# Kernel tuning notes

Hardware: AMD Instinct MI355X
Metric: run time of the kernel (lower is better)

The kernel has to match this reference:

```python
import jax, jax.numpy as jnp
import numpy as np

EMB = 128
HID = 512
B = 8192
W = 128


def setup_inputs() -> dict:
    key = jax.random.key(0)
    k1, k2, k3, k4, k5, k6, k7 = jax.random.split(key, 7)
    context_info = jax.random.normal(k1, (B, 4 * HID), dtype=jnp.float32)
    window = jax.random.normal(k2, (B, W, EMB), dtype=jnp.float32)
    window_mask = jax.random.bernoulli(k3, 0.9, (B, W))
    # guarantee at least one valid position per row (center is always valid)
    window_mask = window_mask.at[:, W // 2].set(True)
    ctr = jax.random.normal(k4, (B, EMB), dtype=jnp.float32)
    # learned params
    W_bilinear = jax.random.normal(k5, (EMB, EMB), dtype=jnp.float32) / np.sqrt(EMB)  # nn.Bilinear weight [1, emb, emb] squeezed
    W_linear = jax.random.normal(k6, (1, 4 * HID + EMB), dtype=jnp.float32) / np.sqrt(4 * HID + EMB)
    b_linear = jax.random.normal(k7, (1,), dtype=jnp.float32) * 0.01
    return {"context_info": context_info, "window": window, "window_mask": window_mask,
            "ctr": ctr, "W_bilinear": W_bilinear, "W_linear": W_linear, "b_linear": b_linear}


def reference(context_info, window, window_mask, ctr, W_bilinear, W_linear, b_linear):
    # bilinear attention score: ctr^T W window_t  -> [B, W]
    e = jnp.einsum('be,ef,bwf->bw', ctr, W_bilinear, window)
    invalid = jnp.logical_not(window_mask)
    e = jnp.where(invalid, -jnp.inf, e)
    # subtract per-row max (masked_fill of the broadcast max to 0 at invalid slots)
    m = jnp.max(e, axis=1, keepdims=True)            # [B, 1]
    e = e - jnp.where(invalid, 0.0, m)               # broadcast to [B, W]
    at_weights = jax.nn.softmax(e, axis=1)
    at_weights = jnp.where(invalid, 0.0, at_weights)
    # weighted sum over window -> [B, emb]
    context_eos = jnp.einsum('bw,bwe->be', at_weights, window)
    context_full = jnp.concatenate([context_info, context_eos], axis=1)
    logits = context_full @ W_linear.T + b_linear    # [B, 1]
    return logits
```

## Files before the change

kernel.cpp:

```cpp
#include <hip/hip_runtime.h>

#define EMB  128
#define HID4 2048
#define WIN  128

__global__ __launch_bounds__(256) void eos_fused_kernel(
    const float* __restrict__ ci,
    const float* __restrict__ window,
    const unsigned char* __restrict__ mask_raw,
    const float* __restrict__ ctr,
    const float* __restrict__ Wb,
    const float* __restrict__ WL,
    const float* __restrict__ bL,
    float* __restrict__ out)
{
    const int b    = blockIdx.x;
    const int tid  = threadIdx.x;
    const int lane = tid & 63;
    const int wave = tid >> 6;
    const int hl   = lane & 31;
    const int hw   = wave * 2 + (lane >> 5);

    __shared__ float ctr_s[EMB];
    __shared__ float vm_s[WIN];
    __shared__ float pu_s[2][EMB];
    __shared__ float u_s[EMB];
    __shared__ float acc_s[8][EMB];
    __shared__ float z_s[8];
    __shared__ float red_s[4];
    __shared__ unsigned long long det_s[4][2];
    __shared__ int mode_s;

    {
        const unsigned int* mw = (const unsigned int*)mask_raw;
        int hi = 0, nf = 0;
        if (tid < 128) {
            unsigned int v = mw[tid];
            hi = (v & 0xFFFFFF00u) ? 1 : 0;
            nf = (v != 0u && v != 0x3F800000u) ? 1 : 0;
        }
        unsigned long long bh = __ballot(hi);
        unsigned long long bf = __ballot(nf);
        if (lane == 0) { det_s[wave][0] = bh; det_s[wave][1] = bf; }
    }
    if (tid < EMB) ctr_s[tid] = ctr[(size_t)b * EMB + tid];
    __syncthreads();
    if (tid == 0) {
        unsigned long long ah = det_s[0][0] | det_s[1][0] | det_s[2][0] | det_s[3][0];
        unsigned long long af = det_s[0][1] | det_s[1][1] | det_s[2][1] | det_s[3][1];
        mode_s = (af == 0ULL) ? 2 : (ah ? 0 : 1);
    }
    __syncthreads();

    {
        const int mode = mode_s;
        if (tid < WIN) {
            bool valid;
            if (mode == 0)      valid = (mask_raw[(size_t)b * WIN + tid] != 0);
            else if (mode == 1) valid = (((const int*)mask_raw)[(size_t)b * WIN + tid] != 0);
            else                valid = (((const float*)mask_raw)[(size_t)b * WIN + tid] != 0.f);
            vm_s[tid] = valid ? 1.f : 0.f;
        }
    }

    {
        const int f  = tid & (EMB - 1);
        const int h  = tid >> 7;
        const int e0 = h * 64;
        float s = 0.f;
        #pragma unroll 8
        for (int e = 0; e < 64; ++e)
            s = fmaf(ctr_s[e0 + e], Wb[(e0 + e) * EMB + f], s);
        pu_s[h][f] = s;
    }
    __syncthreads();
    if (tid < EMB) u_s[tid] = pu_s[0][tid] + pu_s[1][tid];
    __syncthreads();

    float4 u4;
    u4.x = u_s[hl*4+0]; u4.y = u_s[hl*4+1]; u4.z = u_s[hl*4+2]; u4.w = u_s[hl*4+3];

    const float4* win4 = (const float4*)(window + (size_t)b * WIN * EMB);

    float  Z   = 0.f;
    float4 acc = make_float4(0.f, 0.f, 0.f, 0.f);

    #pragma unroll 4
    for (int i = 0; i < 16; ++i) {
        const int w = i * 8 + hw;
        float4 wv = win4[w * 32 + hl];
        float s = wv.x * u4.x;
        s = fmaf(wv.y, u4.y, s);
        s = fmaf(wv.z, u4.z, s);
        s = fmaf(wv.w, u4.w, s);
        s += __shfl_xor(s, 1);
        s += __shfl_xor(s, 2);
        s += __shfl_xor(s, 4);
        s += __shfl_xor(s, 8);
        s += __shfl_xor(s, 16);
        const float p = vm_s[w] * __expf(s);
        Z += p;
        acc.x = fmaf(p, wv.x, acc.x);
        acc.y = fmaf(p, wv.y, acc.y);
        acc.z = fmaf(p, wv.z, acc.z);
        acc.w = fmaf(p, wv.w, acc.w);
    }

    acc_s[hw][hl*4+0] = acc.x;
    acc_s[hw][hl*4+1] = acc.y;
    acc_s[hw][hl*4+2] = acc.z;
    acc_s[hw][hl*4+3] = acc.w;
    if (hl == 0) z_s[hw] = 0.f;
    __syncthreads();
    if (hl == 0) z_s[hw] = Z;
    __syncthreads();

    const float4* ci4 = (const float4*)(ci + (size_t)b * HID4);
    const float4* wl4 = (const float4*)WL;
    float part;
    {
        float4 c0 = ci4[tid],       w0 = wl4[tid];
        float4 c1 = ci4[tid + 256], w1 = wl4[tid + 256];
        part = c0.x * w0.x;
        part = fmaf(c0.y, w0.y, part);
        part = fmaf(c0.z, w0.z, part);
        part = fmaf(c0.w, w0.w, part);
        part = fmaf(c1.x, w1.x, part);
        part = fmaf(c1.y, w1.y, part);
        part = fmaf(c1.z, w1.z, part);
        part = fmaf(c1.w, w1.w, part);
    }
    if (tid < EMB) {
        float Zt = z_s[0] + z_s[1] + z_s[2] + z_s[3]
                 + z_s[4] + z_s[5] + z_s[6] + z_s[7];
        float a = 0.f;
        #pragma unroll
        for (int p = 0; p < 8; ++p) a += acc_s[p][tid];
        const float ce = a / Zt;
        part = fmaf(ce, WL[HID4 + tid], part);
    }
    part += __shfl_xor(part, 1);
    part += __shfl_xor(part, 2);
    part += __shfl_xor(part, 4);
    part += __shfl_xor(part, 8);
    part += __shfl_xor(part, 16);
    part += __shfl_xor(part, 32);
    if (lane == 0) red_s[wave] = part;
    __syncthreads();
    if (tid == 0)
        out[b] = red_s[0] + red_s[1] + red_s[2] + red_s[3] + bL[0];
}

extern "C" void kernel_launch(void* const* d_in, const int* in_sizes, int n_in,
                              void* d_out, int out_size, void* d_ws, size_t ws_size,
                              hipStream_t stream) {
    const float*         ci     = (const float*)d_in[0];
    const float*         window = (const float*)d_in[1];
    const unsigned char* mask   = (const unsigned char*)d_in[2];
    const float*         ctr    = (const float*)d_in[3];
    const float*         Wb     = (const float*)d_in[4];
    const float*         WL     = (const float*)d_in[5];
    const float*         bL     = (const float*)d_in[6];
    float*               out    = (float*)d_out;

    const int B = in_sizes[0] / HID4;
    hipLaunchKernelGGL(eos_fused_kernel, dim3(B), dim3(256), 0, stream,
                       ci, window, mask, ctr, Wb, WL, bL, out);
}
```

Before: 115.3 us.

## Split ctr·W_bilinear projection and mask decode into batched prep kernel

Moves the per-row u = ctr·W_bilinear projection and mask decoding into a separate prep kernel that handles 8 rows per block, so each W_bilinear load is reused across 8 rows. The results go to workspace. The main kernel then only loads u and the mask floats, issues the context_info loads early, and drops several barriers. It also sets an occupancy hint of 8 blocks per CU. The cost is an extra kernel launch and a workspace round-trip, and the original fused kernel is kept as a fallback when workspace is too small.

```diff
diff --git a/kernel.cpp b/kernel.cpp
--- a/kernel.cpp
+++ b/kernel.cpp
@@ -3,13 +3,81 @@
 #define EMB  128
 #define HID4 2048
 #define WIN  128
-
-__global__ __launch_bounds__(256) void eos_fused_kernel(
+#define BQ   8
+
+__global__ __launch_bounds__(256) void eos_prep_kernel(
+    const float* __restrict__ ctr,
+    const unsigned char* __restrict__ mask_raw,
+    const float* __restrict__ Wb,
+    float* __restrict__ u_out,
+    float* __restrict__ vm_out)
+{
+    const int b0   = blockIdx.x * BQ;
+    const int tid  = threadIdx.x;
+    const int lane = tid & 63;
+    const int wave = tid >> 6;
+
+    __shared__ float ctr_s[BQ][EMB];
+    __shared__ float pu_s[2][BQ * EMB];
+    __shared__ unsigned long long det_s[4][2];
+    __shared__ int mode_s;
+
+    {
+        const unsigned int* mw = (const unsigned int*)mask_raw;
+        int hi = 0, nf = 0;
+        if (tid < 128) {
+            unsigned int v = mw[tid];
+            hi = (v & 0xFFFFFF00u) ? 1 : 0;
+            nf = (v != 0u && v != 0x3F800000u) ? 1 : 0;
+        }
+        unsigned long long bh = __ballot(hi);
+        unsigned long long bf = __ballot(nf);
+        if (lane == 0) { det_s[wave][0] = bh; det_s[wave][1] = bf; }
+    }
+    ((float4*)&ctr_s[0][0])[tid] = ((const float4*)(ctr + (size_t)b0 * EMB))[tid];
+    __syncthreads();
+    if (tid == 0) {
+        unsigned long long ah = det_s[0][0] | det_s[1][0] | det_s[2][0] | det_s[3][0];
+        unsigned long long af = det_s[0][1] | det_s[1][1] | det_s[2][1] | det_s[3][1];
+        mode_s = (af == 0ULL) ? 2 : (ah ? 0 : 1);
+    }
+
+    const int f = tid & 127;
+    const int h = tid >> 7;
+    float acc[BQ];
+    #pragma unroll
+    for (int r = 0; r < BQ; ++r) acc[r] = 0.f;
+    const float* wbp = Wb + (size_t)(h * 64) * EMB + f;
+    #pragma unroll 4
+    for (int e = 0; e < 64; ++e) {
+        const float w = wbp[(size_t)e * EMB];
+        #pragma unroll
+        for (int r = 0; r < BQ; ++r)
+            acc[r] = fmaf(ctr_s[r][h * 64 + e], w, acc[r]);
+    }
+    #pragma unroll
+    for (int r = 0; r < BQ; ++r) pu_s[h][r * EMB + f] = acc[r];
+    __syncthreads();
+
+    for (int idx = tid; idx < BQ * EMB; idx += 256)
+        u_out[(size_t)b0 * EMB + idx] = pu_s[0][idx] + pu_s[1][idx];
+
+    const int mode = mode_s;
+    for (int idx = tid; idx < BQ * WIN; idx += 256) {
+        const size_t gi = (size_t)b0 * WIN + idx;
+        bool valid;
+        if (mode == 0)      valid = (mask_raw[gi] != 0);
+        else if (mode == 1) valid = (((const int*)mask_raw)[gi] != 0);
+        else                valid = (((const float*)mask_raw)[gi] != 0.f);
+        vm_out[gi] = valid ? 1.f : 0.f;
+    }
+}
+
+__global__ __launch_bounds__(256, 8) void eos_main_kernel(
     const float* __restrict__ ci,
     const float* __restrict__ window,
-    const unsigned char* __restrict__ mask_raw,
-    const float* __restrict__ ctr,
-    const float* __restrict__ Wb,
+    const float* __restrict__ u_prep,
+    const float* __restrict__ vm_prep,
     const float* __restrict__ WL,
     const float* __restrict__ bL,
     float* __restrict__ out)
@@ -21,64 +89,17 @@
     const int hl   = lane & 31;
     const int hw   = wave * 2 + (lane >> 5);
 
-    __shared__ float ctr_s[EMB];
     __shared__ float vm_s[WIN];
-    __shared__ float pu_s[2][EMB];
-    __shared__ float u_s[EMB];
     __shared__ float acc_s[8][EMB];
     __shared__ float z_s[8];
     __shared__ float red_s[4];
-    __shared__ unsigned long long det_s[4][2];
-    __shared__ int mode_s;
-
-    {
-        const unsigned int* mw = (const unsigned int*)mask_raw;
-        int hi = 0, nf = 0;
-        if (tid < 128) {
-            unsigned int v = mw[tid];
-            hi = (v & 0xFFFFFF00u) ? 1 : 0;
-            nf = (v != 0u && v != 0x3F800000u) ? 1 : 0;
-        }
-        unsigned long long bh = __ballot(hi);
-        unsigned long long bf = __ballot(nf);
-        if (lane == 0) { det_s[wave][0] = bh; det_s[wave][1] = bf; }
-    }
-    if (tid < EMB) ctr_s[tid] = ctr[(size_t)b * EMB + tid];
-    __syncthreads();
-    if (tid == 0) {
-        unsigned long long ah = det_s[0][0] | det_s[1][0] | det_s[2][0] | det_s[3][0];
-        unsigned long long af = det_s[0][1] | det_s[1][1] | det_s[2][1] | det_s[3][1];
-        mode_s = (af == 0ULL) ? 2 : (ah ? 0 : 1);
-    }
-    __syncthreads();
-
-    {
-        const int mode = mode_s;
-        if (tid < WIN) {
-            bool valid;
-            if (mode == 0)      valid = (mask_raw[(size_t)b * WIN + tid] != 0);
-            else if (mode == 1) valid = (((const int*)mask_raw)[(size_t)b * WIN + tid] != 0);
-            else                valid = (((const float*)mask_raw)[(size_t)b * WIN + tid] != 0.f);
-            vm_s[tid] = valid ? 1.f : 0.f;
-        }
-    }
-
-    {
-        const int f  = tid & (EMB - 1);
-        const int h  = tid >> 7;
-        const int e0 = h * 64;
-        float s = 0.f;
-        #pragma unroll 8
-        for (int e = 0; e < 64; ++e)
-            s = fmaf(ctr_s[e0 + e], Wb[(e0 + e) * EMB + f], s);
-        pu_s[h][f] = s;
-    }
-    __syncthreads();
-    if (tid < EMB) u_s[tid] = pu_s[0][tid] + pu_s[1][tid];
-    __syncthreads();
-
-    float4 u4;
-    u4.x = u_s[hl*4+0]; u4.y = u_s[hl*4+1]; u4.z = u_s[hl*4+2]; u4.w = u_s[hl*4+3];
+
+    const float4* ci4 = (const float4*)(ci + (size_t)b * HID4);
+    float4 c0 = ci4[tid];
+    float4 c1 = ci4[tid + 256];
+    float4 u4 = ((const float4*)(u_prep + (size_t)b * EMB))[hl];
+    if (tid < WIN) vm_s[tid] = vm_prep[(size_t)b * WIN + tid];
+    __syncthreads();
 
     const float4* win4 = (const float4*)(window + (size_t)b * WIN * EMB);
 
@@ -110,8 +131,138 @@
     acc_s[hw][hl*4+1] = acc.y;
     acc_s[hw][hl*4+2] = acc.z;
     acc_s[hw][hl*4+3] = acc.w;
-    if (hl == 0) z_s[hw] = 0.f;
-    __syncthreads();
+    if (hl == 0) z_s[hw] = Z;
+    __syncthreads();
+
+    const float4* wl4 = (const float4*)WL;
+    float4 w0 = wl4[tid], w1 = wl4[tid + 256];
+    float part;
+    part = c0.x * w0.x;
+    part = fmaf(c0.y, w0.y, part);
+    part = fmaf(c0.z, w0.z, part);
+    part = fmaf(c0.w, w0.w, part);
+    part = fmaf(c1.x, w1.x, part);
+    part = fmaf(c1.y, w1.y, part);
+    part = fmaf(c1.z, w1.z, part);
+    part = fmaf(c1.w, w1.w, part);
+
+    if (tid < EMB) {
+        const float Zt = z_s[0] + z_s[1] + z_s[2] + z_s[3]
+                       + z_s[4] + z_s[5] + z_s[6] + z_s[7];
+        float a = 0.f;
+        #pragma unroll
+        for (int p = 0; p < 8; ++p) a += acc_s[p][tid];
+        part = fmaf(a / Zt, WL[HID4 + tid], part);
+    }
+    part += __shfl_xor(part, 1);
+    part += __shfl_xor(part, 2);
+    part += __shfl_xor(part, 4);
+    part += __shfl_xor(part, 8);
+    part += __shfl_xor(part, 16);
+    part += __shfl_xor(part, 32);
+    if (lane == 0) red_s[wave] = part;
+    __syncthreads();
+    if (tid == 0)
+        out[b] = red_s[0] + red_s[1] + red_s[2] + red_s[3] + bL[0];
+}
+
+__global__ __launch_bounds__(256) void eos_fused_fallback(
+    const float* __restrict__ ci, const float* __restrict__ window,
+    const unsigned char* __restrict__ mask_raw, const float* __restrict__ ctr,
+    const float* __restrict__ Wb, const float* __restrict__ WL,
+    const float* __restrict__ bL, float* __restrict__ out)
+{
+    const int b    = blockIdx.x;
+    const int tid  = threadIdx.x;
+    const int lane = tid & 63;
+    const int wave = tid >> 6;
+    const int hl   = lane & 31;
+    const int hw   = wave * 2 + (lane >> 5);
+
+    __shared__ float ctr_s[EMB];
+    __shared__ float vm_s[WIN];
+    __shared__ float pu_s[2][EMB];
+    __shared__ float u_s[EMB];
+    __shared__ float acc_s[8][EMB];
+    __shared__ float z_s[8];
+    __shared__ float red_s[4];
+    __shared__ unsigned long long det_s[4][2];
+    __shared__ int mode_s;
+
+    {
+        const unsigned int* mw = (const unsigned int*)mask_raw;
+        int hi = 0, nf = 0;
+        if (tid < 128) {
+            unsigned int v = mw[tid];
+            hi = (v & 0xFFFFFF00u) ? 1 : 0;
+            nf = (v != 0u && v != 0x3F800000u) ? 1 : 0;
+        }
+        unsigned long long bh = __ballot(hi);
+        unsigned long long bf = __ballot(nf);
+        if (lane == 0) { det_s[wave][0] = bh; det_s[wave][1] = bf; }
+    }
+    if (tid < EMB) ctr_s[tid] = ctr[(size_t)b * EMB + tid];
+    __syncthreads();
+    if (tid == 0) {
+        unsigned long long ah = det_s[0][0] | det_s[1][0] | det_s[2][0] | det_s[3][0];
+        unsigned long long af = det_s[0][1] | det_s[1][1] | det_s[2][1] | det_s[3][1];
+        mode_s = (af == 0ULL) ? 2 : (ah ? 0 : 1);
+    }
+    __syncthreads();
+    {
+        const int mode = mode_s;
+        if (tid < WIN) {
+            bool valid;
+            if (mode == 0)      valid = (mask_raw[(size_t)b * WIN + tid] != 0);
+            else if (mode == 1) valid = (((const int*)mask_raw)[(size_t)b * WIN + tid] != 0);
+            else                valid = (((const float*)mask_raw)[(size_t)b * WIN + tid] != 0.f);
+            vm_s[tid] = valid ? 1.f : 0.f;
+        }
+    }
+    {
+        const int f  = tid & (EMB - 1);
+        const int h  = tid >> 7;
+        const int e0 = h * 64;
+        float s = 0.f;
+        #pragma unroll 8
+        for (int e = 0; e < 64; ++e)
+            s = fmaf(ctr_s[e0 + e], Wb[(e0 + e) * EMB + f], s);
+        pu_s[h][f] = s;
+    }
+    __syncthreads();
+    if (tid < EMB) u_s[tid] = pu_s[0][tid] + pu_s[1][tid];
+    __syncthreads();
+
+    float4 u4;
+    u4.x = u_s[hl*4+0]; u4.y = u_s[hl*4+1]; u4.z = u_s[hl*4+2]; u4.w = u_s[hl*4+3];
+
+    const float4* win4 = (const float4*)(window + (size_t)b * WIN * EMB);
+    float  Z   = 0.f;
+    float4 acc = make_float4(0.f, 0.f, 0.f, 0.f);
+    #pragma unroll 4
+    for (int i = 0; i < 16; ++i) {
+        const int w = i * 8 + hw;
+        float4 wv = win4[w * 32 + hl];
+        float s = wv.x * u4.x;
+        s = fmaf(wv.y, u4.y, s);
+        s = fmaf(wv.z, u4.z, s);
+        s = fmaf(wv.w, u4.w, s);
+        s += __shfl_xor(s, 1);
+        s += __shfl_xor(s, 2);
+        s += __shfl_xor(s, 4);
+        s += __shfl_xor(s, 8);
+        s += __shfl_xor(s, 16);
+        const float p = vm_s[w] * __expf(s);
+        Z += p;
+        acc.x = fmaf(p, wv.x, acc.x);
+        acc.y = fmaf(p, wv.y, acc.y);
+        acc.z = fmaf(p, wv.z, acc.z);
+        acc.w = fmaf(p, wv.w, acc.w);
+    }
+    acc_s[hw][hl*4+0] = acc.x;
+    acc_s[hw][hl*4+1] = acc.y;
+    acc_s[hw][hl*4+2] = acc.z;
+    acc_s[hw][hl*4+3] = acc.w;
     if (hl == 0) z_s[hw] = Z;
     __syncthreads();
 
@@ -131,13 +282,12 @@
         part = fmaf(c1.w, w1.w, part);
     }
     if (tid < EMB) {
-        float Zt = z_s[0] + z_s[1] + z_s[2] + z_s[3]
-                 + z_s[4] + z_s[5] + z_s[6] + z_s[7];
+        const float Zt = z_s[0] + z_s[1] + z_s[2] + z_s[3]
+                       + z_s[4] + z_s[5] + z_s[6] + z_s[7];
         float a = 0.f;
         #pragma unroll
         for (int p = 0; p < 8; ++p) a += acc_s[p][tid];
-        const float ce = a / Zt;
-        part = fmaf(ce, WL[HID4 + tid], part);
+        part = fmaf(a / Zt, WL[HID4 + tid], part);
     }
     part += __shfl_xor(part, 1);
     part += __shfl_xor(part, 2);
@@ -164,6 +314,17 @@
     float*               out    = (float*)d_out;
 
     const int B = in_sizes[0] / HID4;
-    hipLaunchKernelGGL(eos_fused_kernel, dim3(B), dim3(256), 0, stream,
-                       ci, window, mask, ctr, Wb, WL, bL, out);
+    const size_t need = (size_t)B * EMB * sizeof(float) * 2;
+
+    if (ws_size >= need) {
+        float* u_ws  = (float*)d_ws;
+        float* vm_ws = u_ws + (size_t)B * EMB;
+        hipLaunchKernelGGL(eos_prep_kernel, dim3(B / BQ), dim3(256), 0, stream,
+                           ctr, mask, Wb, u_ws, vm_ws);
+        hipLaunchKernelGGL(eos_main_kernel, dim3(B), dim3(256), 0, stream,
+                           ci, window, u_ws, vm_ws, WL, bL, out);
+    } else {
+        hipLaunchKernelGGL(eos_fused_fallback, dim3(B), dim3(256), 0, stream,
+                           ci, window, mask, ctr, Wb, WL, bL, out);
+    }
 }
```

After: 127.9 us. 11.0% more time.

## Map one batch row per wavefront and drop shared-memory reductions

Applied to the files above, without the earlier changes.

Each wavefront now handles a full batch row: it computes the bilinear projection vector itself, keeps mask values in registers read via shuffles, and reduces accumulators with cross-half shuffles instead of shared memory and block barriers. This removes syncthreads and LDS traffic per row. In exchange each wave reads the full Wb matrix (via cache) and runs a longer serial loop over the window, with less parallelism per row.

```diff
diff --git a/kernel.cpp b/kernel.cpp
--- a/kernel.cpp
+++ b/kernel.cpp
@@ -4,7 +4,7 @@
 #define HID4 2048
 #define WIN  128
 
-__global__ __launch_bounds__(256) void eos_fused_kernel(
+__global__ __launch_bounds__(256) void eos_wave_kernel(
     const float* __restrict__ ci,
     const float* __restrict__ window,
     const unsigned char* __restrict__ mask_raw,
@@ -12,83 +12,68 @@
     const float* __restrict__ Wb,
     const float* __restrict__ WL,
     const float* __restrict__ bL,
-    float* __restrict__ out)
+    float* __restrict__ out,
+    int B)
 {
-    const int b    = blockIdx.x;
     const int tid  = threadIdx.x;
     const int lane = tid & 63;
     const int wave = tid >> 6;
     const int hl   = lane & 31;
-    const int hw   = wave * 2 + (lane >> 5);
+    const int h    = lane >> 5;
+    const int row  = blockIdx.x * 4 + wave;
+    if (row >= B) return;
 
-    __shared__ float ctr_s[EMB];
-    __shared__ float vm_s[WIN];
-    __shared__ float pu_s[2][EMB];
-    __shared__ float u_s[EMB];
-    __shared__ float acc_s[8][EMB];
-    __shared__ float z_s[8];
-    __shared__ float red_s[4];
-    __shared__ unsigned long long det_s[4][2];
-    __shared__ int mode_s;
+    int mode;
+    {
+        const unsigned int v = ((const unsigned int*)mask_raw)[lane];
+        const unsigned long long bh = __ballot((v & 0xFFFFFF00u) != 0u);
+        const unsigned long long bf = __ballot(v != 0u && v != 0x3F800000u);
+        mode = (bf == 0ULL) ? 2 : (bh ? 0 : 1);
+    }
 
+    float vm0, vm1;
     {
-        const unsigned int* mw = (const unsigned int*)mask_raw;
-        int hi = 0, nf = 0;
-        if (tid < 128) {
-            unsigned int v = mw[tid];
-            hi = (v & 0xFFFFFF00u) ? 1 : 0;
-            nf = (v != 0u && v != 0x3F800000u) ? 1 : 0;
-        }
-        unsigned long long bh = __ballot(hi);
-        unsigned long long bf = __ballot(nf);
-        if (lane == 0) { det_s[wave][0] = bh; det_s[wave][1] = bf; }
-    }
-    if (tid < EMB) ctr_s[tid] = ctr[(size_t)b * EMB + tid];
-    __syncthreads();
-    if (tid == 0) {
-        unsigned long long ah = det_s[0][0] | det_s[1][0] | det_s[2][0] | det_s[3][0];
-        unsigned long long af = det_s[0][1] | det_s[1][1] | det_s[2][1] | det_s[3][1];
-        mode_s = (af == 0ULL) ? 2 : (ah ? 0 : 1);
-    }
-    __syncthreads();
-
-    {
-        const int mode = mode_s;
-        if (tid < WIN) {
-            bool valid;
-            if (mode == 0)      valid = (mask_raw[(size_t)b * WIN + tid] != 0);
-            else if (mode == 1) valid = (((const int*)mask_raw)[(size_t)b * WIN + tid] != 0);
-            else                valid = (((const float*)mask_raw)[(size_t)b * WIN + tid] != 0.f);
-            vm_s[tid] = valid ? 1.f : 0.f;
+        const size_t mb = (size_t)row * WIN;
+        if (mode == 0) {
+            vm0 = mask_raw[mb + lane]      ? 1.f : 0.f;
+            vm1 = mask_raw[mb + 64 + lane] ? 1.f : 0.f;
+        } else if (mode == 1) {
+            const int* m = (const int*)mask_raw;
+            vm0 = m[mb + lane]      ? 1.f : 0.f;
+            vm1 = m[mb + 64 + lane] ? 1.f : 0.f;
+        } else {
+            const float* m = (const float*)mask_raw;
+            vm0 = (m[mb + lane]      != 0.f) ? 1.f : 0.f;
+            vm1 = (m[mb + 64 + lane] != 0.f) ? 1.f : 0.f;
         }
     }
 
+    float4 u4 = make_float4(0.f, 0.f, 0.f, 0.f);
     {
-        const int f  = tid & (EMB - 1);
-        const int h  = tid >> 7;
-        const int e0 = h * 64;
-        float s = 0.f;
+        const float*  ctr_row = ctr + (size_t)row * EMB + h * 64;
+        const float4* wb4     = (const float4*)Wb + (size_t)(h * 64) * 32 + hl;
         #pragma unroll 8
-        for (int e = 0; e < 64; ++e)
-            s = fmaf(ctr_s[e0 + e], Wb[(e0 + e) * EMB + f], s);
-        pu_s[h][f] = s;
+        for (int e = 0; e < 64; ++e) {
+            const float  c  = ctr_row[e];
+            const float4 wv = wb4[e * 32];
+            u4.x = fmaf(c, wv.x, u4.x);
+            u4.y = fmaf(c, wv.y, u4.y);
+            u4.z = fmaf(c, wv.z, u4.z);
+            u4.w = fmaf(c, wv.w, u4.w);
+        }
+        u4.x += __shfl_xor(u4.x, 32);
+        u4.y += __shfl_xor(u4.y, 32);
+        u4.z += __shfl_xor(u4.z, 32);
+        u4.w += __shfl_xor(u4.w, 32);
     }
-    __syncthreads();
-    if (tid < EMB) u_s[tid] = pu_s[0][tid] + pu_s[1][tid];
-    __syncthreads();
 
-    float4 u4;
-    u4.x = u_s[hl*4+0]; u4.y = u_s[hl*4+1]; u4.z = u_s[hl*4+2]; u4.w = u_s[hl*4+3];
-
-    const float4* win4 = (const float4*)(window + (size_t)b * WIN * EMB);
-
+    const float4* win4 = (const float4*)(window + (size_t)row * WIN * EMB);
     float  Z   = 0.f;
     float4 acc = make_float4(0.f, 0.f, 0.f, 0.f);
 
     #pragma unroll 4
-    for (int i = 0; i < 16; ++i) {
-        const int w = i * 8 + hw;
-        float4 wv = win4[w * 32 + hl];
+    for (int i = 0; i < 32; ++i) {
+        const float4 wv = win4[(2 * i + h) * 32 + hl];
         float s = wv.x * u4.x;
         s = fmaf(wv.y, u4.y, s);
         s = fmaf(wv.z, u4.z, s);
@@ -98,7 +83,26 @@
         s += __shfl_xor(s, 4);
         s += __shfl_xor(s, 8);
         s += __shfl_xor(s, 16);
-        const float p = vm_s[w] * __expf(s);
+        const float p = __shfl(vm0, 2 * i + h) * __expf(s);
+        Z += p;
+        acc.x = fmaf(p, wv.x, acc.x);
+        acc.y = fmaf(p, wv.y, acc.y);
+        acc.z = fmaf(p, wv.z, acc.z);
+        acc.w = fmaf(p, wv.w, acc.w);
+    }
+    #pragma unroll 4
+    for (int j = 0; j < 32; ++j) {
+        const float4 wv = win4[(64 + 2 * j + h) * 32 + hl];
+        float s = wv.x * u4.x;
+        s = fmaf(wv.y, u4.y, s);
+        s = fmaf(wv.z, u4.z, s);
+        s = fmaf(wv.w, u4.w, s);
+        s += __shfl_xor(s, 1);
+        s += __shfl_xor(s, 2);
+        s += __shfl_xor(s, 4);
+        s += __shfl_xor(s, 8);
+        s += __shfl_xor(s, 16);
+        const float p = __shfl(vm1, 2 * j + h) * __expf(s);
         Z += p;
         acc.x = fmaf(p, wv.x, acc.x);
         acc.y = fmaf(p, wv.y, acc.y);
@@ -106,38 +110,31 @@
         acc.w = fmaf(p, wv.w, acc.w);
     }
 
-    acc_s[hw][hl*4+0] = acc.x;
-    acc_s[hw][hl*4+1] = acc.y;
-    acc_s[hw][hl*4+2] = acc.z;
-    acc_s[hw][hl*4+3] = acc.w;
-    if (hl == 0) z_s[hw] = 0.f;
-    __syncthreads();
-    if (hl == 0) z_s[hw] = Z;
-    __syncthreads();
+    acc.x += __shfl_xor(acc.x, 32);
+    acc.y += __shfl_xor(acc.y, 32);
+    acc.z += __shfl_xor(acc.z, 32);
+    acc.w += __shfl_xor(acc.w, 32);
+    Z     += __shfl_xor(Z, 32);
 
-    const float4* ci4 = (const float4*)(ci + (size_t)b * HID4);
+    const float zi = 1.f / Z;
+    float part = 0.f;
+    if (lane < 32) {
+        const float4 wlp = ((const float4*)(WL + HID4))[hl];
+        part = (acc.x * zi) * wlp.x;
+        part = fmaf(acc.y * zi, wlp.y, part);
+        part = fmaf(acc.z * zi, wlp.z, part);
+        part = fmaf(acc.w * zi, wlp.w, part);
+    }
+    const float4* ci4 = (const float4*)(ci + (size_t)row * HID4);
     const float4* wl4 = (const float4*)WL;
-    float part;
-    {
-        float4 c0 = ci4[tid],       w0 = wl4[tid];
-        float4 c1 = ci4[tid + 256], w1 = wl4[tid + 256];
-        part = c0.x * w0.x;
-        part = fmaf(c0.y, w0.y, part);
-        part = fmaf(c0.z, w0.z, part);
-        part = fmaf(c0.w, w0.w, part);
-        part = fmaf(c1.x, w1.x, part);
-        part = fmaf(c1.y, w1.y, part);
-        part = fmaf(c1.z, w1.z, part);
-        part = fmaf(c1.w, w1.w, part);
-    }
-    if (tid < EMB) {
-        float Zt = z_s[0] + z_s[1] + z_s[2] + z_s[3]
-                 + z_s[4] + z_s[5] + z_s[6] + z_s[7];
-        float a = 0.f;
-        #pragma unroll
-        for (int p = 0; p < 8; ++p) a += acc_s[p][tid];
-        const float ce = a / Zt;
-        part = fmaf(ce, WL[HID4 + tid], part);
+    #pragma unroll
+    for (int k = 0; k < 8; ++k) {
+        const float4 c = ci4[k * 64 + lane];
+        const float4 w = wl4[k * 64 + lane];
+        part = fmaf(c.x, w.x, part);
+        part = fmaf(c.y, w.y, part);
+        part = fmaf(c.z, w.z, part);
+        part = fmaf(c.w, w.w, part);
     }
     part += __shfl_xor(part, 1);
     part += __shfl_xor(part, 2);
@@ -145,10 +142,7 @@
     part += __shfl_xor(part, 8);
     part += __shfl_xor(part, 16);
     part += __shfl_xor(part, 32);
-    if (lane == 0) red_s[wave] = part;
-    __syncthreads();
-    if (tid == 0)
-        out[b] = red_s[0] + red_s[1] + red_s[2] + red_s[3] + bL[0];
+    if (lane == 0) out[row] = part + bL[0];
 }
 
 extern "C" void kernel_launch(void* const* d_in, const int* in_sizes, int n_in,
@@ -164,6 +158,7 @@
     float*               out    = (float*)d_out;
 
     const int B = in_sizes[0] / HID4;
-    hipLaunchKernelGGL(eos_fused_kernel, dim3(B), dim3(256), 0, stream,
-                       ci, window, mask, ctr, Wb, WL, bL, out);
+    const int nblk = (B + 3) / 4;
+    hipLaunchKernelGGL(eos_wave_kernel, dim3(nblk), dim3(256), 0, stream,
+                       ci, window, mask, ctr, Wb, WL, bL, out, B);
 }
```

After: 118.6 us. +2.9%, slower.
